# Kernel tuning notes

Measured on AMD Instinct MI355X. Metric: run time of the kernel, lower is better.

## Reference

```python
import jax, jax.numpy as jnp
import numpy as np

BATCH = 1_000_000
NUM_KDE = 500_000
RKHS = 20
OUT = 128
NUM_NODES = 100_000


def setup_inputs() -> dict:
    key = jax.random.key(0)
    ks = jax.random.split(key, 9)
    src = jax.random.randint(ks[0], (BATCH,), 0, NUM_NODES, dtype=jnp.int64 if jax.config.read('jax_enable_x64') else jnp.int32)
    dst = jax.random.randint(ks[1], (BATCH,), 0, NUM_NODES, dtype=src.dtype)
    t_diff = jax.random.uniform(ks[2], (BATCH,), dtype=jnp.float32) * 1000.0
    kde_idx = jax.random.randint(ks[3], (BATCH,), 0, NUM_KDE, dtype=src.dtype)
    kde_mask = jax.random.randint(ks[4], (BATCH,), 0, 2) == 1
    kde_table = jax.random.normal(ks[5], (NUM_KDE, RKHS), dtype=jnp.float32)
    W_proj = jax.random.normal(ks[6], (OUT, RKHS), dtype=jnp.float32) * (1.0 / np.sqrt(RKHS))
    b_proj = jnp.zeros((OUT,), dtype=jnp.float32)
    W_fb = jax.random.normal(ks[7], (OUT, 1), dtype=jnp.float32)
    b_fb = jax.random.normal(ks[8], (OUT,), dtype=jnp.float32)
    return {
        'src': src, 'dst': dst, 't_diff': t_diff,
        'kde_idx': kde_idx, 'kde_mask': kde_mask, 'kde_table': kde_table,
        'W_proj': W_proj, 'b_proj': b_proj, 'W_fb': W_fb, 'b_fb': b_fb,
    }


def reference(src, dst, t_diff, kde_idx, kde_mask, kde_table, W_proj, b_proj, W_fb, b_fb):
    # Gather KDE vectors for every edge (miss rows gather a dummy row, masked out below).
    kde_vecs = kde_table[kde_idx]                       # [B, RKHS]
    # rkhs_projection: Linear(RKHS -> OUT)
    kde_out = jnp.einsum('br,or->bo', kde_vecs, W_proj) + b_proj   # [B, OUT]
    # fallback_encoder: cos(Linear(1 -> OUT))
    fb_out = jnp.cos(t_diff[:, None] * W_fb[:, 0][None, :] + b_fb)  # [B, OUT]
    return jnp.where(kde_mask[:, None], kde_out, fb_out)
```

## Files before the change

### kernel.cpp

```cpp
#include <hip/hip_runtime.h>
#include <hip/hip_bf16.h>

#define BATCH_N 1000000
#define RKHS_N 20
#define OUT_N 128
#define RPW 16
#define WAVES 4
#define NBLK 1024
#define TOTAL_WAVES (NBLK * WAVES)
#define NGROUPS (BATCH_N / RPW)

__global__ void kde_probe(const unsigned char* __restrict__ mask,
                          const unsigned short* __restrict__ td,
                          unsigned int* __restrict__ cfg)
{
    int i = blockIdx.x * blockDim.x + threadIdx.x;
    unsigned int bits = 0;
    if ((i & 3) != 0 && mask[i] != 0) bits |= 1u;
    if (td[2 * i] & 0x8000u)          bits |= 2u;
    unsigned long long m1 = __ballot(bits & 1u);
    unsigned long long m2 = __ballot(bits & 2u);
    if ((threadIdx.x & 63) == 0) {
        unsigned int v = (m1 ? 1u : 0u) | (m2 ? 2u : 0u);
        if (v) atomicOr(cfg, v);
    }
}

__device__ __forceinline__ float bflo(unsigned int w) {
    return __uint_as_float(w << 16);
}
__device__ __forceinline__ float bfhi(unsigned int w) {
    return __uint_as_float(w & 0xffff0000u);
}

template<bool BF16> struct ChunkSel;
template<> struct ChunkSel<true>  { using T = uint2; };
template<> struct ChunkSel<false> { using T = uint4; };

struct PFS {
    int      i0, i1;
    unsigned m0, m1;
    unsigned mrow;
    unsigned trow;
};

template<bool BF16, bool MASK8>
__device__ __forceinline__ void run_impl(const void* __restrict__ t_diff,
                                         const int* __restrict__ kde_idx,
                                         const void* __restrict__ kde_mask,
                                         const void* __restrict__ kde_table,
                                         const void* __restrict__ W_proj,
                                         const void* __restrict__ b_proj,
                                         const void* __restrict__ W_fb,
                                         const void* __restrict__ b_fb,
                                         void* __restrict__ out,
                                         unsigned int* __restrict__ lds)
{
    constexpr int CH   = BF16 ? 2 : 4;
    constexpr int LDSW = BF16 ? 12 : 20;
    constexpr int WBUF = RPW * LDSW;
    using CT = typename ChunkSel<BF16>::T;

    const int tid  = threadIdx.x;
    const int wave = tid >> 6;
    const int lane = tid & 63;

    float w0[RKHS_N], w1[RKHS_N];
    float bp0, bp1, wf0, wf1, bb0, bb1;
    if constexpr (BF16) {
        const unsigned int* wp = (const unsigned int*)W_proj;
#pragma unroll
        for (int d = 0; d < 10; ++d) {
            unsigned int a = wp[lane * 20 + d];
            unsigned int b = wp[lane * 20 + 10 + d];
            w0[2 * d] = bflo(a); w0[2 * d + 1] = bfhi(a);
            w1[2 * d] = bflo(b); w1[2 * d + 1] = bfhi(b);
        }
        unsigned int v;
        v = ((const unsigned int*)b_proj)[lane]; bp0 = bflo(v); bp1 = bfhi(v);
        v = ((const unsigned int*)W_fb)[lane];   wf0 = bflo(v); wf1 = bfhi(v);
        v = ((const unsigned int*)b_fb)[lane];   bb0 = bflo(v); bb1 = bfhi(v);
    } else {
        const float* wp = (const float*)W_proj;
#pragma unroll
        for (int k = 0; k < RKHS_N; ++k) {
            w0[k] = wp[(2 * lane) * RKHS_N + k];
            w1[k] = wp[(2 * lane + 1) * RKHS_N + k];
        }
        bp0 = ((const float*)b_proj)[2 * lane]; bp1 = ((const float*)b_proj)[2 * lane + 1];
        wf0 = ((const float*)W_fb)[2 * lane];   wf1 = ((const float*)W_fb)[2 * lane + 1];
        bb0 = ((const float*)b_fb)[2 * lane];   bb1 = ((const float*)b_fb)[2 * lane + 1];
    }

    const int  r0  = lane / 5;
    const int  s0  = lane - 5 * r0;
    const int  r1  = (lane + 64) / 5;
    const int  s1  = (lane + 64) - 5 * r1;
    const bool two = lane < 16;

    const unsigned char*  mb   = (const unsigned char*)kde_mask;
    const unsigned int*   mp32 = (const unsigned int*)kde_mask;
    const unsigned short* tp16 = (const unsigned short*)t_diff;
    const float*          tpf  = (const float*)t_diff;
    const CT*             tbl  = (const CT*)kde_table;

    auto load_pf = [&](int g) -> PFS {
        PFS p;
        const int base = g * RPW;
        p.i0 = kde_idx[base + r0];
        p.m0 = MASK8 ? (unsigned)mb[base + r0] : mp32[base + r0];
        p.i1 = 0; p.m1 = 0; p.mrow = 0; p.trow = 0;
        if (two) {
            p.i1 = kde_idx[base + r1];
            p.m1 = MASK8 ? (unsigned)mb[base + r1] : mp32[base + r1];
        }
        if (lane < RPW) {
            p.mrow = MASK8 ? (unsigned)mb[base + lane] : mp32[base + lane];
            if constexpr (BF16)
                p.trow = ((unsigned)tp16[base + lane]) << 16;
            else
                p.trow = __float_as_uint(tpf[base + lane]);
        }
        return p;
    };

    auto load_tbl = [&](const PFS& p, CT& d0, CT& d1) {
        d0 = CT{}; d1 = CT{};
        if (p.m0)        d0 = tbl[(size_t)(unsigned)p.i0 * 5 + s0];
        if (two && p.m1) d1 = tbl[(size_t)(unsigned)p.i1 * 5 + s1];
    };

    auto commit = [&](unsigned int* wl, const PFS& p, const CT& d0, const CT& d1) {
        if (p.m0)        *(CT*)(wl + r0 * LDSW + s0 * CH) = d0;
        if (two && p.m1) *(CT*)(wl + r1 * LDSW + s1 * CH) = d1;
    };

    auto compute = [&](int g, const unsigned int* wl, const PFS& p) {
        const int base = g * RPW;
#pragma unroll
        for (int r = 0; r < RPW; ++r) {
            unsigned m = (unsigned)__builtin_amdgcn_readlane((int)p.mrow, r);
            float rx, ry;
            if (m) {
                float a0 = bp0, a1 = bp1;
                const unsigned int* rowp = wl + r * LDSW;
                if constexpr (BF16) {
                    uint4 q0 = *(const uint4*)(rowp);
                    uint4 q1 = *(const uint4*)(rowp + 4);
                    uint2 q2 = *(const uint2*)(rowp + 8);
                    unsigned int dwv[10] = {q0.x, q0.y, q0.z, q0.w,
                                            q1.x, q1.y, q1.z, q1.w,
                                            q2.x, q2.y};
#pragma unroll
                    for (int d = 0; d < 10; ++d) {
                        float v0 = bflo(dwv[d]), v1 = bfhi(dwv[d]);
                        a0 = fmaf(v0, w0[2 * d], a0);
                        a1 = fmaf(v0, w1[2 * d], a1);
                        a0 = fmaf(v1, w0[2 * d + 1], a0);
                        a1 = fmaf(v1, w1[2 * d + 1], a1);
                    }
                } else {
                    uint4 q[5];
#pragma unroll
                    for (int i5 = 0; i5 < 5; ++i5) q[i5] = *(const uint4*)(rowp + 4 * i5);
                    const unsigned int* dv = (const unsigned int*)q;
#pragma unroll
                    for (int k = 0; k < RKHS_N; ++k) {
                        float v = __uint_as_float(dv[k]);
                        a0 = fmaf(v, w0[k], a0);
                        a1 = fmaf(v, w1[k], a1);
                    }
                }
                rx = a0; ry = a1;
            } else {
                float t = __uint_as_float(
                    (unsigned)__builtin_amdgcn_readlane((int)p.trow, r));
                rx = __cosf(fmaf(t, wf0, bb0));
                ry = __cosf(fmaf(t, wf1, bb1));
            }

            size_t gi = (size_t)(base + r);
            if constexpr (BF16) {
                __hip_bfloat162 pk;
                pk.x = __float2bfloat16(rx);
                pk.y = __float2bfloat16(ry);
                unsigned int ub;
                __builtin_memcpy(&ub, &pk, 4);
                __builtin_nontemporal_store(ub, (unsigned int*)out + gi * 64 + lane);
            } else {
                float2 fv; fv.x = rx; fv.y = ry;
                unsigned long long uv;
                __builtin_memcpy(&uv, &fv, 8);
                __builtin_nontemporal_store(uv, (unsigned long long*)out + gi * 64 + lane);
            }
        }
    };

    unsigned int* wl0 = lds + wave * (2 * WBUF);
    unsigned int* wl1 = wl0 + WBUF;

    int g = blockIdx.x * WAVES + wave;
    PFS cur = load_pf(g);
    CT d0, d1;
    load_tbl(cur, d0, d1);
    commit(wl0, cur, d0, d1);
    int gn = g + TOTAL_WAVES;
    PFS nxt{};
    if (gn < NGROUPS) nxt = load_pf(gn);
    int cb = 0;
    for (;;) {
        const bool have = (gn < NGROUPS);
        if (have) load_tbl(nxt, d0, d1);
        const int gnn = gn + TOTAL_WAVES;
        PFS n2{};
        if (gnn < NGROUPS) n2 = load_pf(gnn);
        compute(g, cb ? wl1 : wl0, cur);
        if (!have) break;
        commit(cb ? wl0 : wl1, nxt, d0, d1);
        cur = nxt; nxt = n2; g = gn; gn = gnn; cb ^= 1;
    }
}

__global__ __launch_bounds__(256)
void kde_main(const void* __restrict__ t_diff,
              const int* __restrict__ kde_idx,
              const void* __restrict__ kde_mask,
              const void* __restrict__ kde_table,
              const void* __restrict__ W_proj,
              const void* __restrict__ b_proj,
              const void* __restrict__ W_fb,
              const void* __restrict__ b_fb,
              void* __restrict__ out,
              const unsigned int* __restrict__ cfg)
{
    __shared__ unsigned int lds[WAVES * 2 * RPW * 20];
    const unsigned int c = *cfg;
    if (c & 2u) {
        if (c & 1u) run_impl<false, true >(t_diff, kde_idx, kde_mask, kde_table, W_proj, b_proj, W_fb, b_fb, out, lds);
        else        run_impl<false, false>(t_diff, kde_idx, kde_mask, kde_table, W_proj, b_proj, W_fb, b_fb, out, lds);
    } else {
        if (c & 1u) run_impl<true,  true >(t_diff, kde_idx, kde_mask, kde_table, W_proj, b_proj, W_fb, b_fb, out, lds);
        else        run_impl<true,  false>(t_diff, kde_idx, kde_mask, kde_table, W_proj, b_proj, W_fb, b_fb, out, lds);
    }
}

extern "C" void kernel_launch(void* const* d_in, const int* in_sizes, int n_in,
                              void* d_out, int out_size, void* d_ws, size_t ws_size,
                              hipStream_t stream)
{
    const void* t_diff    = d_in[2];
    const int*  kde_idx   = (const int*)d_in[3];
    const void* kde_mask  = d_in[4];
    const void* kde_table = d_in[5];
    const void* W_proj    = d_in[6];
    const void* b_proj    = d_in[7];
    const void* W_fb      = d_in[8];
    const void* b_fb      = d_in[9];

    unsigned int* cfg = (unsigned int*)d_ws;
    hipMemsetAsync(cfg, 0, sizeof(unsigned int), stream);
    kde_probe<<<256, 256, 0, stream>>>((const unsigned char*)kde_mask,
                                       (const unsigned short*)t_diff, cfg);
    kde_main<<<NBLK, 256, 0, stream>>>(
        t_diff, kde_idx, kde_mask, kde_table, W_proj, b_proj, W_fb, b_fb,
        d_out, cfg);
}
```

Before: 588.3 us.

## Split f32/bf16 paths into separate kernels with deeper gather prefetch

Splits the single templated kernel into separate f32 and bf16 kernels, both launched, each returning early when the runtime dtype flag does not match. The f32 path gets a three-deep prefetch pipeline with the mask folded into the index (-1 for misses), plus launch bounds of 256 with min 4 blocks. The bf16 kernel gets a smaller LDS footprint. The intent is to cut register and LDS pressure from the combined template and hide gather latency better, at the cost of an extra, mostly empty kernel launch.

```diff
diff --git a/kernel.cpp b/kernel.cpp
--- a/kernel.cpp
+++ b/kernel.cpp
@@ -9,6 +9,8 @@
 #define NBLK 1024
 #define TOTAL_WAVES (NBLK * WAVES)
 #define NGROUPS (BATCH_N / RPW)
+#define STRIDE TOTAL_WAVES
+
 
 __global__ void kde_probe(const unsigned char* __restrict__ mask,
                           const unsigned short* __restrict__ td,
@@ -33,19 +35,182 @@
     return __uint_as_float(w & 0xffff0000u);
 }
 
-template<bool BF16> struct ChunkSel;
-template<> struct ChunkSel<true>  { using T = uint2; };
-template<> struct ChunkSel<false> { using T = uint4; };
-
-struct PFS {
+struct PF32 {
+    int      pi0, pi1;
+    unsigned trow;
+};
+
+template<bool MASK8>
+__device__ __forceinline__ void run_f32(const float* __restrict__ t_diff,
+                                        const int* __restrict__ kde_idx,
+                                        const void* __restrict__ kde_mask,
+                                        const uint4* __restrict__ tbl,
+                                        const float* __restrict__ W_proj,
+                                        const float* __restrict__ b_proj,
+                                        const float* __restrict__ W_fb,
+                                        const float* __restrict__ b_fb,
+                                        void* __restrict__ out,
+                                        unsigned int* __restrict__ lds)
+{
+    constexpr int LDSW = 20;
+    constexpr int WBUF = RPW * LDSW;
+
+    const int tid  = threadIdx.x;
+    const int wave = tid >> 6;
+    const int lane = tid & 63;
+    const int wid  = blockIdx.x * WAVES + wave;
+
+    float w0[RKHS_N], w1[RKHS_N];
+#pragma unroll
+    for (int k = 0; k < RKHS_N; ++k) {
+        w0[k] = W_proj[(2 * lane) * RKHS_N + k];
+        w1[k] = W_proj[(2 * lane + 1) * RKHS_N + k];
+    }
+    const float bp0 = b_proj[2 * lane], bp1 = b_proj[2 * lane + 1];
+    const float wf0 = W_fb[2 * lane],   wf1 = W_fb[2 * lane + 1];
+    const float bb0 = b_fb[2 * lane],   bb1 = b_fb[2 * lane + 1];
+
+    const int  r0  = lane / 5;
+    const int  s0  = lane - 5 * r0;
+    const int  r1  = (lane + 64) / 5;
+    const int  s1  = (lane + 64) - 5 * r1;
+    const bool two = lane < 16;
+
+    const unsigned char* mb = (const unsigned char*)kde_mask;
+    const unsigned int*  mw = (const unsigned int*)kde_mask;
+
+    auto load_pf = [&](int g) -> PF32 {
+        PF32 p;
+        const int base = g * RPW;
+        unsigned m0 = MASK8 ? (unsigned)mb[base + r0] : mw[base + r0];
+        int      i0 = kde_idx[base + r0];
+        p.pi0 = m0 ? i0 : -1;
+        p.pi1 = -1;
+        if (two) {
+            unsigned m1 = MASK8 ? (unsigned)mb[base + r1] : mw[base + r1];
+            int      i1 = kde_idx[base + r1];
+            p.pi1 = m1 ? i1 : -1;
+        }
+        p.trow = (lane < RPW) ? __float_as_uint(t_diff[base + lane]) : 0u;
+        return p;
+    };
+
+    auto load_tbl = [&](const PF32& p, uint4& d0, uint4& d1) {
+        if (p.pi0 >= 0)        d0 = tbl[(size_t)(unsigned)p.pi0 * 5 + s0];
+        if (two && p.pi1 >= 0) d1 = tbl[(size_t)(unsigned)p.pi1 * 5 + s1];
+    };
+
+    auto commit = [&](unsigned int* wl, const PF32& p,
+                      const uint4& d0, const uint4& d1) {
+        if (p.pi0 >= 0)        *(uint4*)(wl + r0 * LDSW + s0 * 4) = d0;
+        if (two && p.pi1 >= 0) *(uint4*)(wl + r1 * LDSW + s1 * 4) = d1;
+    };
+
+    auto compute = [&](int g, const unsigned int* wl, const PF32& p) {
+        const int base = g * RPW;
+#pragma unroll
+        for (int r = 0; r < RPW; ++r) {
+            int pr = (r < 13) ? __builtin_amdgcn_readlane(p.pi0, 5 * r)
+                              : __builtin_amdgcn_readlane(p.pi1, 5 * r - 64);
+            float rx, ry;
+            if (pr >= 0) {
+                float a0 = bp0, a1 = bp1;
+                const unsigned int* rowp = wl + r * LDSW;
+                uint4 q[5];
+#pragma unroll
+                for (int i5 = 0; i5 < 5; ++i5) q[i5] = *(const uint4*)(rowp + 4 * i5);
+                const unsigned int* dv = (const unsigned int*)q;
+#pragma unroll
+                for (int k = 0; k < RKHS_N; ++k) {
+                    float v = __uint_as_float(dv[k]);
+                    a0 = fmaf(v, w0[k], a0);
+                    a1 = fmaf(v, w1[k], a1);
+                }
+                rx = a0; ry = a1;
+            } else {
+                float t = __uint_as_float(
+                    (unsigned)__builtin_amdgcn_readlane((int)p.trow, r));
+                rx = __cosf(fmaf(t, wf0, bb0));
+                ry = __cosf(fmaf(t, wf1, bb1));
+            }
+
+            size_t gi = (size_t)(base + r);
+            float2 fv; fv.x = rx; fv.y = ry;
+            unsigned long long uv;
+            __builtin_memcpy(&uv, &fv, 8);
+            __builtin_nontemporal_store(uv, (unsigned long long*)out + gi * 64 + lane);
+        }
+    };
+
+    unsigned int* L0 = lds + wave * (2 * WBUF);
+    unsigned int* L1 = L0 + WBUF;
+
+    int g = wid;
+    PF32 pc = load_pf(g);
+    PF32 p1 = load_pf(g + STRIDE);
+    PF32 p2 = load_pf(g + 2 * STRIDE);
+    {
+        uint4 t0{}, t1{};
+        load_tbl(pc, t0, t1);
+        commit(L0, pc, t0, t1);
+    }
+    uint4 a0{}, a1{}, b0{}, b1{};
+    load_tbl(p1, a0, a1);
+
+    for (;;) {
+        if (g + 2 * STRIDE < NGROUPS) load_tbl(p2, b0, b1);
+        PF32 p3 = (g + 3 * STRIDE < NGROUPS) ? load_pf(g + 3 * STRIDE)
+                                             : PF32{-1, -1, 0u};
+        compute(g, L0, pc);
+        if (!(g + STRIDE < NGROUPS)) return;
+        commit(L1, p1, a0, a1);
+        pc = p1; p1 = p2; p2 = p3; g += STRIDE;
+
+        if (g + 2 * STRIDE < NGROUPS) load_tbl(p2, a0, a1);
+        PF32 p3b = (g + 3 * STRIDE < NGROUPS) ? load_pf(g + 3 * STRIDE)
+                                              : PF32{-1, -1, 0u};
+        compute(g, L1, pc);
+        if (!(g + STRIDE < NGROUPS)) return;
+        commit(L0, p1, b0, b1);
+        pc = p1; p1 = p2; p2 = p3b; g += STRIDE;
+    }
+}
+
+__global__ __launch_bounds__(256, 4)
+void kde_f32(const void* __restrict__ t_diff,
+             const int* __restrict__ kde_idx,
+             const void* __restrict__ kde_mask,
+             const void* __restrict__ kde_table,
+             const void* __restrict__ W_proj,
+             const void* __restrict__ b_proj,
+             const void* __restrict__ W_fb,
+             const void* __restrict__ b_fb,
+             void* __restrict__ out,
+             const unsigned int* __restrict__ cfg)
+{
+    __shared__ unsigned int lds[WAVES * 2 * RPW * 20];
+    const unsigned int c = *cfg;
+    if (!(c & 2u)) return;
+    if (c & 1u)
+        run_f32<true >((const float*)t_diff, kde_idx, kde_mask,
+                       (const uint4*)kde_table, (const float*)W_proj,
+                       (const float*)b_proj, (const float*)W_fb,
+                       (const float*)b_fb, out, lds);
+    else
+        run_f32<false>((const float*)t_diff, kde_idx, kde_mask,
+                       (const uint4*)kde_table, (const float*)W_proj,
+                       (const float*)b_proj, (const float*)W_fb,
+                       (const float*)b_fb, out, lds);
+}
+
+struct PFB {
     int      i0, i1;
     unsigned m0, m1;
-    unsigned mrow;
-    unsigned trow;
+    unsigned mrow, trow;
 };
 
-template<bool BF16, bool MASK8>
-__device__ __forceinline__ void run_impl(const void* __restrict__ t_diff,
+template<bool MASK8>
+__device__ __forceinline__ void run_bf16(const void* __restrict__ t_diff,
                                          const int* __restrict__ kde_idx,
                                          const void* __restrict__ kde_mask,
                                          const void* __restrict__ kde_table,
@@ -56,10 +221,8 @@
                                          void* __restrict__ out,
                                          unsigned int* __restrict__ lds)
 {
-    constexpr int CH   = BF16 ? 2 : 4;
-    constexpr int LDSW = BF16 ? 12 : 20;
+    constexpr int LDSW = 12;
     constexpr int WBUF = RPW * LDSW;
-    using CT = typename ChunkSel<BF16>::T;
 
     const int tid  = threadIdx.x;
     const int wave = tid >> 6;
@@ -67,7 +230,7 @@
 
     float w0[RKHS_N], w1[RKHS_N];
     float bp0, bp1, wf0, wf1, bb0, bb1;
-    if constexpr (BF16) {
+    {
         const unsigned int* wp = (const unsigned int*)W_proj;
 #pragma unroll
         for (int d = 0; d < 10; ++d) {
@@ -80,16 +243,6 @@
         v = ((const unsigned int*)b_proj)[lane]; bp0 = bflo(v); bp1 = bfhi(v);
         v = ((const unsigned int*)W_fb)[lane];   wf0 = bflo(v); wf1 = bfhi(v);
         v = ((const unsigned int*)b_fb)[lane];   bb0 = bflo(v); bb1 = bfhi(v);
-    } else {
-        const float* wp = (const float*)W_proj;
-#pragma unroll
-        for (int k = 0; k < RKHS_N; ++k) {
-            w0[k] = wp[(2 * lane) * RKHS_N + k];
-            w1[k] = wp[(2 * lane + 1) * RKHS_N + k];
-        }
-        bp0 = ((const float*)b_proj)[2 * lane]; bp1 = ((const float*)b_proj)[2 * lane + 1];
-        wf0 = ((const float*)W_fb)[2 * lane];   wf1 = ((const float*)W_fb)[2 * lane + 1];
-        bb0 = ((const float*)b_fb)[2 * lane];   bb1 = ((const float*)b_fb)[2 * lane + 1];
     }
 
     const int  r0  = lane / 5;
@@ -101,11 +254,10 @@
     const unsigned char*  mb   = (const unsigned char*)kde_mask;
     const unsigned int*   mp32 = (const unsigned int*)kde_mask;
     const unsigned short* tp16 = (const unsigned short*)t_diff;
-    const float*          tpf  = (const float*)t_diff;
-    const CT*             tbl  = (const CT*)kde_table;
-
-    auto load_pf = [&](int g) -> PFS {
-        PFS p;
+    const uint2*          tbl  = (const uint2*)kde_table;
+
+    auto load_pf = [&](int g) -> PFB {
+        PFB p;
         const int base = g * RPW;
         p.i0 = kde_idx[base + r0];
         p.m0 = MASK8 ? (unsigned)mb[base + r0] : mp32[base + r0];
@@ -116,26 +268,24 @@
         }
         if (lane < RPW) {
             p.mrow = MASK8 ? (unsigned)mb[base + lane] : mp32[base + lane];
-            if constexpr (BF16)
-                p.trow = ((unsigned)tp16[base + lane]) << 16;
-            else
-                p.trow = __float_as_uint(tpf[base + lane]);
+            p.trow = ((unsigned)tp16[base + lane]) << 16;
         }
         return p;
     };
 
-    auto load_tbl = [&](const PFS& p, CT& d0, CT& d1) {
-        d0 = CT{}; d1 = CT{};
+    auto load_tbl = [&](const PFB& p, uint2& d0, uint2& d1) {
+        d0 = uint2{}; d1 = uint2{};
         if (p.m0)        d0 = tbl[(size_t)(unsigned)p.i0 * 5 + s0];
         if (two && p.m1) d1 = tbl[(size_t)(unsigned)p.i1 * 5 + s1];
     };
 
-    auto commit = [&](unsigned int* wl, const PFS& p, const CT& d0, const CT& d1) {
-        if (p.m0)        *(CT*)(wl + r0 * LDSW + s0 * CH) = d0;
-        if (two && p.m1) *(CT*)(wl + r1 * LDSW + s1 * CH) = d1;
-    };
-
-    auto compute = [&](int g, const unsigned int* wl, const PFS& p) {
+    auto commit = [&](unsigned int* wl, const PFB& p,
+                      const uint2& d0, const uint2& d1) {
+        if (p.m0)        *(uint2*)(wl + r0 * LDSW + s0 * 2) = d0;
+        if (two && p.m1) *(uint2*)(wl + r1 * LDSW + s1 * 2) = d1;
+    };
+
+    auto compute = [&](int g, const unsigned int* wl, const PFB& p) {
         const int base = g * RPW;
 #pragma unroll
         for (int r = 0; r < RPW; ++r) {
@@ -144,32 +294,19 @@
             if (m) {
                 float a0 = bp0, a1 = bp1;
                 const unsigned int* rowp = wl + r * LDSW;
-                if constexpr (BF16) {
-                    uint4 q0 = *(const uint4*)(rowp);
-                    uint4 q1 = *(const uint4*)(rowp + 4);
-                    uint2 q2 = *(const uint2*)(rowp + 8);
-                    unsigned int dwv[10] = {q0.x, q0.y, q0.z, q0.w,
-                                            q1.x, q1.y, q1.z, q1.w,
-                                            q2.x, q2.y};
-#pragma unroll
-                    for (int d = 0; d < 10; ++d) {
-                        float v0 = bflo(dwv[d]), v1 = bfhi(dwv[d]);
-                        a0 = fmaf(v0, w0[2 * d], a0);
-                        a1 = fmaf(v0, w1[2 * d], a1);
-                        a0 = fmaf(v1, w0[2 * d + 1], a0);
-                        a1 = fmaf(v1, w1[2 * d + 1], a1);
-                    }
-                } else {
-                    uint4 q[5];
-#pragma unroll
-                    for (int i5 = 0; i5 < 5; ++i5) q[i5] = *(const uint4*)(rowp + 4 * i5);
-                    const unsigned int* dv = (const unsigned int*)q;
-#pragma unroll
-                    for (int k = 0; k < RKHS_N; ++k) {
-                        float v = __uint_as_float(dv[k]);
-                        a0 = fmaf(v, w0[k], a0);
-                        a1 = fmaf(v, w1[k], a1);
-                    }
+                uint4 q0 = *(const uint4*)(rowp);
+                uint4 q1 = *(const uint4*)(rowp + 4);
+                uint2 q2 = *(const uint2*)(rowp + 8);
+                unsigned int dwv[10] = {q0.x, q0.y, q0.z, q0.w,
+                                        q1.x, q1.y, q1.z, q1.w,
+                                        q2.x, q2.y};
+#pragma unroll
+                for (int d = 0; d < 10; ++d) {
+                    float v0 = bflo(dwv[d]), v1 = bfhi(dwv[d]);
+                    a0 = fmaf(v0, w0[2 * d], a0);
+                    a1 = fmaf(v0, w1[2 * d], a1);
+                    a0 = fmaf(v1, w0[2 * d + 1], a0);
+                    a1 = fmaf(v1, w1[2 * d + 1], a1);
                 }
                 rx = a0; ry = a1;
             } else {
@@ -180,19 +317,12 @@
             }
 
             size_t gi = (size_t)(base + r);
-            if constexpr (BF16) {
-                __hip_bfloat162 pk;
-                pk.x = __float2bfloat16(rx);
-                pk.y = __float2bfloat16(ry);
-                unsigned int ub;
-                __builtin_memcpy(&ub, &pk, 4);
-                __builtin_nontemporal_store(ub, (unsigned int*)out + gi * 64 + lane);
-            } else {
-                float2 fv; fv.x = rx; fv.y = ry;
-                unsigned long long uv;
-                __builtin_memcpy(&uv, &fv, 8);
-                __builtin_nontemporal_store(uv, (unsigned long long*)out + gi * 64 + lane);
-            }
+            __hip_bfloat162 pk;
+            pk.x = __float2bfloat16(rx);
+            pk.y = __float2bfloat16(ry);
+            unsigned int ub;
+            __builtin_memcpy(&ub, &pk, 4);
+            __builtin_nontemporal_store(ub, (unsigned int*)out + gi * 64 + lane);
         }
     };
 
@@ -200,19 +330,19 @@
     unsigned int* wl1 = wl0 + WBUF;
 
     int g = blockIdx.x * WAVES + wave;
-    PFS cur = load_pf(g);
-    CT d0, d1;
+    PFB cur = load_pf(g);
+    uint2 d0, d1;
     load_tbl(cur, d0, d1);
     commit(wl0, cur, d0, d1);
     int gn = g + TOTAL_WAVES;
-    PFS nxt{};
+    PFB nxt{};
     if (gn < NGROUPS) nxt = load_pf(gn);
     int cb = 0;
     for (;;) {
         const bool have = (gn < NGROUPS);
         if (have) load_tbl(nxt, d0, d1);
         const int gnn = gn + TOTAL_WAVES;
-        PFS n2{};
+        PFB n2{};
         if (gnn < NGROUPS) n2 = load_pf(gnn);
         compute(g, cb ? wl1 : wl0, cur);
         if (!have) break;
@@ -222,7 +352,7 @@
 }
 
 __global__ __launch_bounds__(256)
-void kde_main(const void* __restrict__ t_diff,
+void kde_bf16(const void* __restrict__ t_diff,
               const int* __restrict__ kde_idx,
               const void* __restrict__ kde_mask,
               const void* __restrict__ kde_table,
@@ -233,15 +363,11 @@
               void* __restrict__ out,
               const unsigned int* __restrict__ cfg)
 {
-    __shared__ unsigned int lds[WAVES * 2 * RPW * 20];
+    __shared__ unsigned int lds[WAVES * 2 * RPW * 12];
     const unsigned int c = *cfg;
-    if (c & 2u) {
-        if (c & 1u) run_impl<false, true >(t_diff, kde_idx, kde_mask, kde_table, W_proj, b_proj, W_fb, b_fb, out, lds);
-        else        run_impl<false, false>(t_diff, kde_idx, kde_mask, kde_table, W_proj, b_proj, W_fb, b_fb, out, lds);
-    } else {
-        if (c & 1u) run_impl<true,  true >(t_diff, kde_idx, kde_mask, kde_table, W_proj, b_proj, W_fb, b_fb, out, lds);
-        else        run_impl<true,  false>(t_diff, kde_idx, kde_mask, kde_table, W_proj, b_proj, W_fb, b_fb, out, lds);
-    }
+    if (c & 2u) return;
+    if (c & 1u) run_bf16<true >(t_diff, kde_idx, kde_mask, kde_table, W_proj, b_proj, W_fb, b_fb, out, lds);
+    else        run_bf16<false>(t_diff, kde_idx, kde_mask, kde_table, W_proj, b_proj, W_fb, b_fb, out, lds);
 }
 
 extern "C" void kernel_launch(void* const* d_in, const int* in_sizes, int n_in,
@@ -261,7 +387,10 @@
     hipMemsetAsync(cfg, 0, sizeof(unsigned int), stream);
     kde_probe<<<256, 256, 0, stream>>>((const unsigned char*)kde_mask,
                                        (const unsigned short*)t_diff, cfg);
-    kde_main<<<NBLK, 256, 0, stream>>>(
+    kde_f32<<<NBLK, 256, 0, stream>>>(
         t_diff, kde_idx, kde_mask, kde_table, W_proj, b_proj, W_fb, b_fb,
         d_out, cfg);
-}
+    kde_bf16<<<NBLK, 256, 0, stream>>>(
+        t_diff, kde_idx, kde_mask, kde_table, W_proj, b_proj, W_fb, b_fb,
+        d_out, cfg);
+}
```

Result: no change. 596.9 us (+1.5%).

## Replace LDS-staged fp32 path with per-row register pipeline over contiguous chunks

Applied to the files above, without the earlier changes.

For fp32 inputs, each wave now handles a contiguous chunk of 245 rows. It has every lane load the full 20-float table row directly into registers, with a two-deep software pipeline of metadata and row loads. Both the projection and the cosine fallback are computed branch-free and a select picks the result, which removes the LDS staging, readlane broadcasts and divergent branches. In exchange every lane issues redundant table loads (broadcast across the wave) and always does the cosine and FMA work. The bf16 path is kept but specialized, with a smaller LDS buffer.

```diff
diff --git a/kernel.cpp b/kernel.cpp
--- a/kernel.cpp
+++ b/kernel.cpp
@@ -9,6 +9,7 @@
 #define NBLK 1024
 #define TOTAL_WAVES (NBLK * WAVES)
 #define NGROUPS (BATCH_N / RPW)
+#define CHUNK 245
 
 __global__ void kde_probe(const unsigned char* __restrict__ mask,
                           const unsigned short* __restrict__ td,
@@ -33,19 +34,111 @@
     return __uint_as_float(w & 0xffff0000u);
 }
 
-template<bool BF16> struct ChunkSel;
-template<> struct ChunkSel<true>  { using T = uint2; };
-template<> struct ChunkSel<false> { using T = uint4; };
-
-struct PFS {
+template<bool MASK8>
+__device__ __forceinline__ void run_f32(const float* __restrict__ t_diff,
+                                        const int* __restrict__ kde_idx,
+                                        const void* __restrict__ kde_mask,
+                                        const float* __restrict__ tb,
+                                        const float* __restrict__ W_proj,
+                                        const float* __restrict__ b_proj,
+                                        const float* __restrict__ W_fb,
+                                        const float* __restrict__ b_fb,
+                                        void* __restrict__ out)
+{
+    const int tid  = threadIdx.x;
+    const int wave = tid >> 6;
+    const int lane = tid & 63;
+    const int wid  = blockIdx.x * WAVES + wave;
+
+    const int row0 = wid * CHUNK;
+    if (row0 >= BATCH_N) return;
+    const int rend = (row0 + CHUNK < BATCH_N) ? row0 + CHUNK : BATCH_N;
+
+    float w0[RKHS_N], w1[RKHS_N];
+#pragma unroll
+    for (int k = 0; k < RKHS_N; ++k) {
+        w0[k] = W_proj[(2 * lane) * RKHS_N + k];
+        w1[k] = W_proj[(2 * lane + 1) * RKHS_N + k];
+    }
+    const float bp0 = b_proj[2 * lane], bp1 = b_proj[2 * lane + 1];
+    const float wf0 = W_fb[2 * lane],   wf1 = W_fb[2 * lane + 1];
+    const float bb0 = b_fb[2 * lane],   bb1 = b_fb[2 * lane + 1];
+
+    const unsigned char* mb = (const unsigned char*)kde_mask;
+    const unsigned int*  mw = (const unsigned int*)kde_mask;
+
+    auto ld_meta = [&](int r, int& i, unsigned& m, float& t) {
+        int rc = (r < rend) ? r : (rend - 1);
+        i = kde_idx[rc];
+        m = MASK8 ? (unsigned)mb[rc] : mw[rc];
+        t = t_diff[rc];
+    };
+    auto ld_row = [&](int i, float4& q0, float4& q1, float4& q2,
+                      float4& q3, float4& q4) {
+        const float4* rp = (const float4*)(tb + (size_t)(unsigned)i * RKHS_N);
+        q0 = rp[0]; q1 = rp[1]; q2 = rp[2]; q3 = rp[3]; q4 = rp[4];
+    };
+    auto body = [&](int r, const float4& q0, const float4& q1, const float4& q2,
+                    const float4& q3, const float4& q4, unsigned cm, float ct) {
+        float vv[20];
+        *(float4*)(vv + 0)  = q0;
+        *(float4*)(vv + 4)  = q1;
+        *(float4*)(vv + 8)  = q2;
+        *(float4*)(vv + 12) = q3;
+        *(float4*)(vv + 16) = q4;
+        float a0 = bp0, a1 = bp1;
+#pragma unroll
+        for (int k = 0; k < RKHS_N; ++k) {
+            a0 = fmaf(vv[k], w0[k], a0);
+            a1 = fmaf(vv[k], w1[k], a1);
+        }
+        float fb0 = __cosf(fmaf(ct, wf0, bb0));
+        float fb1 = __cosf(fmaf(ct, wf1, bb1));
+        float rx = cm ? a0 : fb0;
+        float ry = cm ? a1 : fb1;
+        float2 fv; fv.x = rx; fv.y = ry;
+        unsigned long long uv;
+        __builtin_memcpy(&uv, &fv, 8);
+        __builtin_nontemporal_store(uv, (unsigned long long*)out
+                                        + (size_t)r * 64 + lane);
+    };
+
+    int      iA, iB;
+    unsigned mA, mB;
+    float    tA, tB;
+    float4   dA0, dA1, dA2, dA3, dA4, dB0, dB1, dB2, dB3, dB4;
+    unsigned cm;
+    float    ct;
+
+    ld_meta(row0, iA, mA, tA);
+    ld_row(iA, dA0, dA1, dA2, dA3, dA4);
+    ld_meta(row0 + 1, iB, mB, tB);
+    cm = mA; ct = tA;
+
+    int r = row0;
+    for (;;) {
+        ld_meta(r + 2, iA, mA, tA);
+        ld_row(iB, dB0, dB1, dB2, dB3, dB4);
+        body(r, dA0, dA1, dA2, dA3, dA4, cm, ct);
+        cm = mB; ct = tB;
+        ++r; if (r == rend) break;
+
+        ld_meta(r + 2, iB, mB, tB);
+        ld_row(iA, dA0, dA1, dA2, dA3, dA4);
+        body(r, dB0, dB1, dB2, dB3, dB4, cm, ct);
+        cm = mA; ct = tA;
+        ++r; if (r == rend) break;
+    }
+}
+
+struct PFB {
     int      i0, i1;
     unsigned m0, m1;
-    unsigned mrow;
-    unsigned trow;
+    unsigned mrow, trow;
 };
 
-template<bool BF16, bool MASK8>
-__device__ __forceinline__ void run_impl(const void* __restrict__ t_diff,
+template<bool MASK8>
+__device__ __forceinline__ void run_bf16(const void* __restrict__ t_diff,
                                          const int* __restrict__ kde_idx,
                                          const void* __restrict__ kde_mask,
                                          const void* __restrict__ kde_table,
@@ -56,10 +149,8 @@
                                          void* __restrict__ out,
                                          unsigned int* __restrict__ lds)
 {
-    constexpr int CH   = BF16 ? 2 : 4;
-    constexpr int LDSW = BF16 ? 12 : 20;
+    constexpr int LDSW = 12;
     constexpr int WBUF = RPW * LDSW;
-    using CT = typename ChunkSel<BF16>::T;
 
     const int tid  = threadIdx.x;
     const int wave = tid >> 6;
@@ -67,7 +158,7 @@
 
     float w0[RKHS_N], w1[RKHS_N];
     float bp0, bp1, wf0, wf1, bb0, bb1;
-    if constexpr (BF16) {
+    {
         const unsigned int* wp = (const unsigned int*)W_proj;
 #pragma unroll
         for (int d = 0; d < 10; ++d) {
@@ -80,16 +171,6 @@
         v = ((const unsigned int*)b_proj)[lane]; bp0 = bflo(v); bp1 = bfhi(v);
         v = ((const unsigned int*)W_fb)[lane];   wf0 = bflo(v); wf1 = bfhi(v);
         v = ((const unsigned int*)b_fb)[lane];   bb0 = bflo(v); bb1 = bfhi(v);
-    } else {
-        const float* wp = (const float*)W_proj;
-#pragma unroll
-        for (int k = 0; k < RKHS_N; ++k) {
-            w0[k] = wp[(2 * lane) * RKHS_N + k];
-            w1[k] = wp[(2 * lane + 1) * RKHS_N + k];
-        }
-        bp0 = ((const float*)b_proj)[2 * lane]; bp1 = ((const float*)b_proj)[2 * lane + 1];
-        wf0 = ((const float*)W_fb)[2 * lane];   wf1 = ((const float*)W_fb)[2 * lane + 1];
-        bb0 = ((const float*)b_fb)[2 * lane];   bb1 = ((const float*)b_fb)[2 * lane + 1];
     }
 
     const int  r0  = lane / 5;
@@ -101,11 +182,10 @@
     const unsigned char*  mb   = (const unsigned char*)kde_mask;
     const unsigned int*   mp32 = (const unsigned int*)kde_mask;
     const unsigned short* tp16 = (const unsigned short*)t_diff;
-    const float*          tpf  = (const float*)t_diff;
-    const CT*             tbl  = (const CT*)kde_table;
-
-    auto load_pf = [&](int g) -> PFS {
-        PFS p;
+    const uint2*          tbl  = (const uint2*)kde_table;
+
+    auto load_pf = [&](int g) -> PFB {
+        PFB p;
         const int base = g * RPW;
         p.i0 = kde_idx[base + r0];
         p.m0 = MASK8 ? (unsigned)mb[base + r0] : mp32[base + r0];
@@ -116,26 +196,24 @@
         }
         if (lane < RPW) {
             p.mrow = MASK8 ? (unsigned)mb[base + lane] : mp32[base + lane];
-            if constexpr (BF16)
-                p.trow = ((unsigned)tp16[base + lane]) << 16;
-            else
-                p.trow = __float_as_uint(tpf[base + lane]);
+            p.trow = ((unsigned)tp16[base + lane]) << 16;
         }
         return p;
     };
 
-    auto load_tbl = [&](const PFS& p, CT& d0, CT& d1) {
-        d0 = CT{}; d1 = CT{};
+    auto load_tbl = [&](const PFB& p, uint2& d0, uint2& d1) {
+        d0 = uint2{}; d1 = uint2{};
         if (p.m0)        d0 = tbl[(size_t)(unsigned)p.i0 * 5 + s0];
         if (two && p.m1) d1 = tbl[(size_t)(unsigned)p.i1 * 5 + s1];
     };
 
-    auto commit = [&](unsigned int* wl, const PFS& p, const CT& d0, const CT& d1) {
-        if (p.m0)        *(CT*)(wl + r0 * LDSW + s0 * CH) = d0;
-        if (two && p.m1) *(CT*)(wl + r1 * LDSW + s1 * CH) = d1;
-    };
-
-    auto compute = [&](int g, const unsigned int* wl, const PFS& p) {
+    auto commit = [&](unsigned int* wl, const PFB& p,
+                      const uint2& d0, const uint2& d1) {
+        if (p.m0)        *(uint2*)(wl + r0 * LDSW + s0 * 2) = d0;
+        if (two && p.m1) *(uint2*)(wl + r1 * LDSW + s1 * 2) = d1;
+    };
+
+    auto compute = [&](int g, const unsigned int* wl, const PFB& p) {
         const int base = g * RPW;
 #pragma unroll
         for (int r = 0; r < RPW; ++r) {
@@ -144,32 +222,19 @@
             if (m) {
                 float a0 = bp0, a1 = bp1;
                 const unsigned int* rowp = wl + r * LDSW;
-                if constexpr (BF16) {
-                    uint4 q0 = *(const uint4*)(rowp);
-                    uint4 q1 = *(const uint4*)(rowp + 4);
-                    uint2 q2 = *(const uint2*)(rowp + 8);
-                    unsigned int dwv[10] = {q0.x, q0.y, q0.z, q0.w,
-                                            q1.x, q1.y, q1.z, q1.w,
-                                            q2.x, q2.y};
-#pragma unroll
-                    for (int d = 0; d < 10; ++d) {
-                        float v0 = bflo(dwv[d]), v1 = bfhi(dwv[d]);
-                        a0 = fmaf(v0, w0[2 * d], a0);
-                        a1 = fmaf(v0, w1[2 * d], a1);
-                        a0 = fmaf(v1, w0[2 * d + 1], a0);
-                        a1 = fmaf(v1, w1[2 * d + 1], a1);
-                    }
-                } else {
-                    uint4 q[5];
-#pragma unroll
-                    for (int i5 = 0; i5 < 5; ++i5) q[i5] = *(const uint4*)(rowp + 4 * i5);
-                    const unsigned int* dv = (const unsigned int*)q;
-#pragma unroll
-                    for (int k = 0; k < RKHS_N; ++k) {
-                        float v = __uint_as_float(dv[k]);
-                        a0 = fmaf(v, w0[k], a0);
-                        a1 = fmaf(v, w1[k], a1);
-                    }
+                uint4 q0 = *(const uint4*)(rowp);
+                uint4 q1 = *(const uint4*)(rowp + 4);
+                uint2 q2 = *(const uint2*)(rowp + 8);
+                unsigned int dwv[10] = {q0.x, q0.y, q0.z, q0.w,
+                                        q1.x, q1.y, q1.z, q1.w,
+                                        q2.x, q2.y};
+#pragma unroll
+                for (int d = 0; d < 10; ++d) {
+                    float v0 = bflo(dwv[d]), v1 = bfhi(dwv[d]);
+                    a0 = fmaf(v0, w0[2 * d], a0);
+                    a1 = fmaf(v0, w1[2 * d], a1);
+                    a0 = fmaf(v1, w0[2 * d + 1], a0);
+                    a1 = fmaf(v1, w1[2 * d + 1], a1);
                 }
                 rx = a0; ry = a1;
             } else {
@@ -180,19 +245,12 @@
             }
 
             size_t gi = (size_t)(base + r);
-            if constexpr (BF16) {
-                __hip_bfloat162 pk;
-                pk.x = __float2bfloat16(rx);
-                pk.y = __float2bfloat16(ry);
-                unsigned int ub;
-                __builtin_memcpy(&ub, &pk, 4);
-                __builtin_nontemporal_store(ub, (unsigned int*)out + gi * 64 + lane);
-            } else {
-                float2 fv; fv.x = rx; fv.y = ry;
-                unsigned long long uv;
-                __builtin_memcpy(&uv, &fv, 8);
-                __builtin_nontemporal_store(uv, (unsigned long long*)out + gi * 64 + lane);
-            }
+            __hip_bfloat162 pk;
+            pk.x = __float2bfloat16(rx);
+            pk.y = __float2bfloat16(ry);
+            unsigned int ub;
+            __builtin_memcpy(&ub, &pk, 4);
+            __builtin_nontemporal_store(ub, (unsigned int*)out + gi * 64 + lane);
         }
     };
 
@@ -200,19 +258,19 @@
     unsigned int* wl1 = wl0 + WBUF;
 
     int g = blockIdx.x * WAVES + wave;
-    PFS cur = load_pf(g);
-    CT d0, d1;
+    PFB cur = load_pf(g);
+    uint2 d0, d1;
     load_tbl(cur, d0, d1);
     commit(wl0, cur, d0, d1);
     int gn = g + TOTAL_WAVES;
-    PFS nxt{};
+    PFB nxt{};
     if (gn < NGROUPS) nxt = load_pf(gn);
     int cb = 0;
     for (;;) {
         const bool have = (gn < NGROUPS);
         if (have) load_tbl(nxt, d0, d1);
         const int gnn = gn + TOTAL_WAVES;
-        PFS n2{};
+        PFB n2{};
         if (gnn < NGROUPS) n2 = load_pf(gnn);
         compute(g, cb ? wl1 : wl0, cur);
         if (!have) break;
@@ -233,14 +291,22 @@
               void* __restrict__ out,
               const unsigned int* __restrict__ cfg)
 {
-    __shared__ unsigned int lds[WAVES * 2 * RPW * 20];
+    __shared__ unsigned int lds[WAVES * 2 * RPW * 12];
     const unsigned int c = *cfg;
     if (c & 2u) {
-        if (c & 1u) run_impl<false, true >(t_diff, kde_idx, kde_mask, kde_table, W_proj, b_proj, W_fb, b_fb, out, lds);
-        else        run_impl<false, false>(t_diff, kde_idx, kde_mask, kde_table, W_proj, b_proj, W_fb, b_fb, out, lds);
+        if (c & 1u)
+            run_f32<true >((const float*)t_diff, kde_idx, kde_mask,
+                           (const float*)kde_table, (const float*)W_proj,
+                           (const float*)b_proj, (const float*)W_fb,
+                           (const float*)b_fb, out);
+        else
+            run_f32<false>((const float*)t_diff, kde_idx, kde_mask,
+                           (const float*)kde_table, (const float*)W_proj,
+                           (const float*)b_proj, (const float*)W_fb,
+                           (const float*)b_fb, out);
     } else {
-        if (c & 1u) run_impl<true,  true >(t_diff, kde_idx, kde_mask, kde_table, W_proj, b_proj, W_fb, b_fb, out, lds);
-        else        run_impl<true,  false>(t_diff, kde_idx, kde_mask, kde_table, W_proj, b_proj, W_fb, b_fb, out, lds);
+        if (c & 1u) run_bf16<true >(t_diff, kde_idx, kde_mask, kde_table, W_proj, b_proj, W_fb, b_fb, out, lds);
+        else        run_bf16<false>(t_diff, kde_idx, kde_mask, kde_table, W_proj, b_proj, W_fb, b_fb, out, lds);
     }
 }
 
```

After: 739.6 us. 1.26x slower.
